# Optimization experiments

Hardware: AMD Instinct MI355X
Metric: run time of the kernel (lower is better)

The kernel has to match this reference:

```python
import jax, jax.numpy as jnp
import numpy as np

N = 50000
NEG_SLOPE = 0.2

def _gat_layer(x, src, dst, W, a_src, a_dst, b):
    # x: [N, Fin], W: [Fin, Fout], a_src/a_dst: [Fout], b: [Fout]
    h = x @ W                                  # [N, Fout]
    alpha_src = h @ a_src                      # [N]
    alpha_dst = h @ a_dst                      # [N]
    e = alpha_src[src] + alpha_dst[dst]        # [E]
    e = jnp.where(e > 0, e, NEG_SLOPE * e)     # leaky_relu
    # segment softmax over incoming edges of each dst node
    m = jax.ops.segment_max(e, dst, num_segments=N)
    w = jnp.exp(e - m[dst])
    denom = jax.ops.segment_sum(w, dst, num_segments=N) + jnp.asarray(1e-16, e.dtype)
    alpha = w / denom[dst]                     # [E]
    out = jax.ops.segment_sum(alpha[:, None] * h[src], dst, num_segments=N)
    return out + b

def setup_inputs() -> dict:
    key = jax.random.key(0)
    ks = jax.random.split(key, 10)
    x = jax.random.normal(ks[0], (N, 128), dtype=jnp.float32)
    edge_index = jax.random.randint(ks[1], (2, 800000), 0, N, dtype=jnp.int64)
    def glorot(k, shape):
        fan = shape[0] + (shape[1] if len(shape) > 1 else 1)
        s = jnp.sqrt(6.0 / fan)
        return jax.random.uniform(k, shape, jnp.float32, -s, s)
    return {
        "x": x,
        "edge_index": edge_index,
        "W1": glorot(ks[2], (128, 64)),
        "a1_src": glorot(ks[3], (64,)),
        "a1_dst": glorot(ks[4], (64,)),
        "b1": jnp.zeros((64,), jnp.float32),
        "W2": glorot(ks[5], (64, 64)),
        "a2_src": glorot(ks[6], (64,)),
        "a2_dst": glorot(ks[7], (64,)),
        "b2": jnp.zeros((64,), jnp.float32),
    }

def reference(x, edge_index, W1, a1_src, a1_dst, b1, W2, a2_src, a2_dst, b2):
    loops = jnp.arange(N, dtype=edge_index.dtype)
    src = jnp.concatenate([edge_index[0], loops])  # add self-loops (PyG default)
    dst = jnp.concatenate([edge_index[1], loops])
    h = _gat_layer(x, src, dst, W1, a1_src, a1_dst, b1)
    h = jax.nn.relu(h)
    out = _gat_layer(h, src, dst, W2, a2_src, a2_dst, b2)
    return out
```

## Files before the change

### kernel.cpp

```cpp
#include <hip/hip_runtime.h>
#include <hip/hip_bf16.h>
#include <hip/hip_fp16.h>
#include <cstddef>


#define NNODES 50000
#define NEDGES 800000
#define FOUT   64
#define NBKT   512
#define BSPAN  98
#define CHUNK  8192
#define REGS   2560
#define NLBMAX 128

__device__ __forceinline__ float leaky(float t) { return t > 0.f ? t : 0.2f * t; }
#define RL(v, j) __builtin_amdgcn_readlane((v), (j))


__global__ __launch_bounds__(256) void k_localsort(
    const int* __restrict__ ei, unsigned* __restrict__ gout,
    int* __restrict__ goff, int E)
{
    __shared__ unsigned lrec[CHUNK];
    __shared__ unsigned lsrt[CHUNK];
    __shared__ int cnt[NBKT];
    __shared__ int cur[NBKT];
    __shared__ int exc[NBKT + 1];

    const int t = threadIdx.x;
    const int blk = blockIdx.x;
    const int e0 = blk * CHUNK;
    const int e1 = min(e0 + CHUNK, E);
    const int ne = e1 - e0;

    for (int i = t; i < NBKT; i += 256) cnt[i] = 0;
    __syncthreads();

    for (int i = e0 + t; i < e1; i += 256) {
        unsigned s = (unsigned)ei[i];
        unsigned d = (unsigned)ei[E + i];
        lrec[i - e0] = s | (d << 16);
        atomicAdd(&cnt[d / BSPAN], 1);
    }
    __syncthreads();

    if (t < 64) {
        int c[8]; int s = 0;
        #pragma unroll
        for (int k = 0; k < 8; ++k) { c[k] = cnt[t * 8 + k]; s += c[k]; }
        int inc = s;
        #pragma unroll
        for (int d = 1; d < 64; d <<= 1) { int u = __shfl_up(inc, d); if (t >= d) inc += u; }
        int ex = inc - s;
        #pragma unroll
        for (int k = 0; k < 8; ++k) { exc[t * 8 + k] = ex; cur[t * 8 + k] = ex; ex += c[k]; }
        if (t == 63) exc[NBKT] = ex;
    }
    __syncthreads();

    for (int i = t; i < ne; i += 256) {
        unsigned r = lrec[i];
        unsigned d = r >> 16;
        unsigned b = d / BSPAN;
        int p = atomicAdd(&cur[b], 1);
        lsrt[p] = (r & 0xFFFFu) | ((d - b * BSPAN) << 16);
    }
    __syncthreads();

    for (int i = t; i < ne; i += 256) gout[e0 + i] = lsrt[i];
    for (int i = t; i < NBKT + 1; i += 256)
        goff[blk * (NBKT + 1) + i] = e0 + exc[i];
}


__global__ __launch_bounds__(256) void k_csr_bucket(
    const unsigned* __restrict__ gout, const int* __restrict__ goff,
    int* __restrict__ csrc, int* __restrict__ rowstart, int* __restrict__ rowend,
    int n, int nlb)
{
    __shared__ unsigned ltmp[REGS];
    __shared__ int lout[REGS];
    __shared__ int lcnt[BSPAN];
    __shared__ int lbase[BSPAN + 1];
    __shared__ int lcur[BSPAN];
    __shared__ int rg0[NLBMAX];
    __shared__ int rbase[NLBMAX + 1];

    const int t = threadIdx.x;
    const int bkt = blockIdx.x;
    const int node0 = bkt * BSPAN;
    if (node0 >= n) return;
    const int nn = min(BSPAN, n - node0);

    for (int i = t; i < BSPAN; i += 256) lcnt[i] = (i < nn) ? 1 : 0;
    __shared__ int rlen[NLBMAX];
    if (t < nlb) {
        int g0 = goff[t * (NBKT + 1) + bkt];
        int g1 = goff[t * (NBKT + 1) + bkt + 1];
        rg0[t] = g0;
        rlen[t] = g1 - g0;
    }
    __syncthreads();

    if (t < 64) {
        int b0 = t * 2, b1 = t * 2 + 1;
        int c0 = (b0 < nlb) ? rlen[b0] : 0;
        int c1 = (b1 < nlb) ? rlen[b1] : 0;
        int s = c0 + c1;
        int inc = s;
        #pragma unroll
        for (int d = 1; d < 64; d <<= 1) { int u = __shfl_up(inc, d); if (t >= d) inc += u; }
        int ex = inc - s;
        rbase[b0] = ex;
        if (b1 <= NLBMAX) rbase[b1] = ex + c0;
        if (t == 63) rbase[nlb] = inc;
    }
    __syncthreads();

    const int tot = min(rbase[nlb], REGS - BSPAN);

    for (int i = t; i < tot; i += 256) {
        int lo = 0, hi = nlb;
        while (hi - lo > 1) {
            int mid = (lo + hi) >> 1;
            if (rbase[mid] <= i) lo = mid; else hi = mid;
        }
        ltmp[i] = gout[rg0[lo] + (i - rbase[lo])];
    }
    __syncthreads();

    for (int i = t; i < tot; i += 256) atomicAdd(&lcnt[ltmp[i] >> 16], 1);
    __syncthreads();

    if (t < 64) {
        int b0 = t * 2, b1 = t * 2 + 1;
        int c0 = (b0 < BSPAN) ? lcnt[b0] : 0;
        int c1 = (b1 < BSPAN) ? lcnt[b1] : 0;
        int s = c0 + c1;
        int inc = s;
        #pragma unroll
        for (int d = 1; d < 64; d <<= 1) { int u = __shfl_up(inc, d); if (t >= d) inc += u; }
        int ex = inc - s;
        if (b0 < BSPAN) { lbase[b0] = ex;      lcur[b0] = ex + 1; }
        if (b1 < BSPAN) { lbase[b1] = ex + c0; lcur[b1] = ex + c0 + 1; }
        if (t == 63) lbase[BSPAN] = inc;
    }
    __syncthreads();

    for (int i = t; i < nn; i += 256) lout[lbase[i]] = node0 + i;
    for (int i = t; i < tot; i += 256) {
        unsigned r = ltmp[i];
        int p = atomicAdd(&lcur[r >> 16], 1);
        lout[p] = (int)(r & 0xFFFFu);
    }
    __syncthreads();

    const int gbase = bkt * REGS;
    const int total = tot + nn;
    for (int i = t; i < total; i += 256) csrc[gbase + i] = lout[i];
    for (int i = t; i < nn; i += 256) {
        rowstart[node0 + i] = gbase + lbase[i];
        rowend[node0 + i]   = gbase + lbase[i + 1];
    }
}


template <int K>
__global__ __launch_bounds__(256) void gemm_alpha(
    const float* __restrict__ x, const float* __restrict__ W,
    const float* __restrict__ a_src, const float* __restrict__ a_dst,
    __half* __restrict__ h16, float* __restrict__ as_, float* __restrict__ ad_, int n)
{
    __shared__ __align__(16) float Ws[K * 64];
    __shared__ __align__(16) float xT[K * 64];
    __shared__ float red_s[4][64];
    __shared__ float red_d[4][64];

    const int t = threadIdx.x;
    const int lane = t & 63;
    const int wv = t >> 6;
    const int rg = lane & 15;
    const int cg = lane >> 4;
    const int r0 = blockIdx.x * 64;
    const int c0 = wv * 16 + cg * 4;

    {
        const float4* Wg = (const float4*)W;
        float4* Wl = (float4*)Ws;
        for (int i = t; i < K * 16; i += 256) Wl[i] = Wg[i];
    }
    for (int i = t; i < 16 * K; i += 256) {
        int r = i & 63;
        int kq = i >> 6;
        int row = r0 + r;
        float4 v = make_float4(0.f, 0.f, 0.f, 0.f);
        if (row < n) v = ((const float4*)(x + (size_t)row * K))[kq];
        xT[(kq * 4 + 0) * 64 + r] = v.x;
        xT[(kq * 4 + 1) * 64 + r] = v.y;
        xT[(kq * 4 + 2) * 64 + r] = v.z;
        xT[(kq * 4 + 3) * 64 + r] = v.w;
    }
    __syncthreads();

    float acc[4][4];
    #pragma unroll
    for (int i = 0; i < 4; ++i)
        #pragma unroll
        for (int j = 0; j < 4; ++j) acc[i][j] = 0.f;

    #pragma unroll 4
    for (int k = 0; k < K; ++k) {
        float4 xa = *(const float4*)&xT[k * 64 + rg * 4];
        float4 wb = *(const float4*)&Ws[k * 64 + c0];
        acc[0][0] = fmaf(xa.x, wb.x, acc[0][0]);
        acc[0][1] = fmaf(xa.x, wb.y, acc[0][1]);
        acc[0][2] = fmaf(xa.x, wb.z, acc[0][2]);
        acc[0][3] = fmaf(xa.x, wb.w, acc[0][3]);
        acc[1][0] = fmaf(xa.y, wb.x, acc[1][0]);
        acc[1][1] = fmaf(xa.y, wb.y, acc[1][1]);
        acc[1][2] = fmaf(xa.y, wb.z, acc[1][2]);
        acc[1][3] = fmaf(xa.y, wb.w, acc[1][3]);
        acc[2][0] = fmaf(xa.z, wb.x, acc[2][0]);
        acc[2][1] = fmaf(xa.z, wb.y, acc[2][1]);
        acc[2][2] = fmaf(xa.z, wb.z, acc[2][2]);
        acc[2][3] = fmaf(xa.z, wb.w, acc[2][3]);
        acc[3][0] = fmaf(xa.w, wb.x, acc[3][0]);
        acc[3][1] = fmaf(xa.w, wb.y, acc[3][1]);
        acc[3][2] = fmaf(xa.w, wb.z, acc[3][2]);
        acc[3][3] = fmaf(xa.w, wb.w, acc[3][3]);
    }

    #pragma unroll
    for (int i = 0; i < 4; ++i) {
        int row = r0 + rg * 4 + i;
        if (row < n) {
            __half2 p0 = __floats2half2_rn(acc[i][0], acc[i][1]);
            __half2 p1 = __floats2half2_rn(acc[i][2], acc[i][3]);
            int2 pk;
            pk.x = *(int*)&p0;
            pk.y = *(int*)&p1;
            *(int2*)(h16 + (size_t)row * 64 + c0) = pk;
        }
    }

    float a_s[4], a_d[4];
    #pragma unroll
    for (int j = 0; j < 4; ++j) { a_s[j] = a_src[c0 + j]; a_d[j] = a_dst[c0 + j]; }
    #pragma unroll
    for (int i = 0; i < 4; ++i) {
        float pa = acc[i][0] * a_s[0] + acc[i][1] * a_s[1] + acc[i][2] * a_s[2] + acc[i][3] * a_s[3];
        float pd = acc[i][0] * a_d[0] + acc[i][1] * a_d[1] + acc[i][2] * a_d[2] + acc[i][3] * a_d[3];
        pa += __shfl_xor(pa, 16); pa += __shfl_xor(pa, 32);
        pd += __shfl_xor(pd, 16); pd += __shfl_xor(pd, 32);
        if (cg == 0) { red_s[wv][rg * 4 + i] = pa; red_d[wv][rg * 4 + i] = pd; }
    }
    __syncthreads();
    if (t < 64) {
        int row = r0 + t;
        if (row < n) {
            as_[row] = red_s[0][t] + red_s[1][t] + red_s[2][t] + red_s[3][t];
            ad_[row] = red_d[0][t] + red_d[1][t] + red_d[2][t] + red_d[3][t];
        }
    }
}


template <bool RELU>
__device__ __forceinline__ void agg_one(
    int node, int lane, int2* __restrict__ swrow,
    const int* __restrict__ rowstart, const int* __restrict__ rowend,
    const int* __restrict__ csrc, const __half* __restrict__ h16,
    const float* __restrict__ as_, const float* __restrict__ ad_,
    const float* __restrict__ bias, float* __restrict__ out)
{
    const int start = rowstart[node];
    const int end   = rowend[node];
    const int deg   = end - start;
    const float adn = ad_[node];

    if (deg <= 64) {
        int s = 0;
        float e = -1e30f;
        if (lane < deg) {
            s = csrc[start + lane];
            e = leaky(as_[s] + adn);
        }
        float m = e;
        #pragma unroll
        for (int d = 32; d >= 1; d >>= 1) m = fmaxf(m, __shfl_xor(m, d));
        float w = (lane < deg) ? __expf(e - m) : 0.f;
        float dsum = w;
        #pragma unroll
        for (int d = 32; d >= 1; d >>= 1) dsum += __shfl_xor(dsum, d);

        swrow[lane] = make_int2(s << 6, __float_as_int(w));

        const int g  = lane >> 3;
        const int fl = (lane & 7) << 3;
        const __half* __restrict__ hf = h16 + fl;
        const int niter = (deg + 7) >> 3;

        int2 sw[8];
        uint4 v[8];
        #pragma unroll
        for (int j = 0; j < 8; ++j) {
            if (j < niter) {
                sw[j] = swrow[(j << 3) + g];
                v[j] = *(const uint4*)(hf + sw[j].x);
            }
        }
        float af[8] = {0.f, 0.f, 0.f, 0.f, 0.f, 0.f, 0.f, 0.f};
        #pragma unroll
        for (int j = 0; j < 8; ++j) {
            if (j < niter) {
                float wj = __int_as_float(sw[j].y);
                unsigned uu[4] = {v[j].x, v[j].y, v[j].z, v[j].w};
                #pragma unroll
                for (int q = 0; q < 4; ++q) {
                    __half2 h2 = *(__half2*)&uu[q];
                    float2 f2 = __half22float2(h2);
                    af[2 * q]     = fmaf(wj, f2.x, af[2 * q]);
                    af[2 * q + 1] = fmaf(wj, f2.y, af[2 * q + 1]);
                }
            }
        }
        #pragma unroll
        for (int q = 0; q < 8; ++q) {
            af[q] += __shfl_xor(af[q], 8);
            af[q] += __shfl_xor(af[q], 16);
            af[q] += __shfl_xor(af[q], 32);
        }
        if (g == 0) {
            float inv = 1.f / dsum;
            float* op = out + (size_t)node * 64 + fl;
            float4 b0 = *(const float4*)(bias + fl);
            float4 b1 = *(const float4*)(bias + fl + 4);
            float4 o0, o1;
            o0.x = fmaf(af[0], inv, b0.x); o0.y = fmaf(af[1], inv, b0.y);
            o0.z = fmaf(af[2], inv, b0.z); o0.w = fmaf(af[3], inv, b0.w);
            o1.x = fmaf(af[4], inv, b1.x); o1.y = fmaf(af[5], inv, b1.y);
            o1.z = fmaf(af[6], inv, b1.z); o1.w = fmaf(af[7], inv, b1.w);
            if (RELU) {
                o0.x = fmaxf(o0.x, 0.f); o0.y = fmaxf(o0.y, 0.f);
                o0.z = fmaxf(o0.z, 0.f); o0.w = fmaxf(o0.w, 0.f);
                o1.x = fmaxf(o1.x, 0.f); o1.y = fmaxf(o1.y, 0.f);
                o1.z = fmaxf(o1.z, 0.f); o1.w = fmaxf(o1.w, 0.f);
            }
            *(float4*)op = o0;
            *(float4*)(op + 4) = o1;
        }
    } else {
        const __half* __restrict__ hp = h16 + lane;
        float m = -1e30f;
        for (int base = start; base < end; base += 64) {
            int idx = base + lane;
            if (idx < end) m = fmaxf(m, leaky(as_[csrc[idx]] + adn));
        }
        #pragma unroll
        for (int d = 32; d >= 1; d >>= 1) m = fmaxf(m, __shfl_xor(m, d));

        float acc0 = 0.f, acc1 = 0.f, acc2 = 0.f, acc3 = 0.f, dsum = 0.f;
        for (int base = start; base < end; base += 64) {
            int idx = base + lane;
            int s = 0; float w = 0.f;
            if (idx < end) {
                s = csrc[idx];
                w = __expf(leaky(as_[s] + adn) - m);
            }
            dsum += w;
            int off = s << 6;
            int wu = __float_as_uint(w);
            int cnt = min(64, end - base);
            int cr = (cnt + 3) & ~3;
            for (int j = 0; j < cr; j += 4) {
                int   o0 = RL(off, j + 0), o1 = RL(off, j + 1);
                int   o2 = RL(off, j + 2), o3 = RL(off, j + 3);
                float w0 = __uint_as_float(RL(wu, j + 0));
                float w1 = __uint_as_float(RL(wu, j + 1));
                float w2 = __uint_as_float(RL(wu, j + 2));
                float w3 = __uint_as_float(RL(wu, j + 3));
                float v0 = __half2float(hp[o0]), v1 = __half2float(hp[o1]);
                float v2 = __half2float(hp[o2]), v3 = __half2float(hp[o3]);
                acc0 = fmaf(w0, v0, acc0);
                acc1 = fmaf(w1, v1, acc1);
                acc2 = fmaf(w2, v2, acc2);
                acc3 = fmaf(w3, v3, acc3);
            }
        }
        #pragma unroll
        for (int d = 32; d >= 1; d >>= 1) dsum += __shfl_xor(dsum, d);
        float acc = (acc0 + acc1) + (acc2 + acc3);
        float o = acc / dsum + bias[lane];
        if (RELU) o = fmaxf(o, 0.f);
        out[(size_t)node * 64 + lane] = o;
    }
}

template <bool RELU>
__global__ __launch_bounds__(256) void k_aggregate(
    const int* __restrict__ rowstart, const int* __restrict__ rowend,
    const int* __restrict__ csrc,
    const __half* __restrict__ h16, const float* __restrict__ as_,
    const float* __restrict__ ad_, const float* __restrict__ bias,
    float* __restrict__ out, int n)
{
    __shared__ int2 swL[4][64];

    const int lane = threadIdx.x & 63;
    const int wid  = threadIdx.x >> 6;
    const int nodeA = (blockIdx.x * 4 + wid) * 2;
    if (nodeA >= n) return;

    const int half = lane >> 5;
    const int hl   = lane & 31;
    const int node = nodeA + half;

    const int start = rowstart[node];
    const int end   = rowend[node];
    const int deg   = end - start;
    const int mdeg  = max(deg, __shfl_xor(deg, 32));

    if (mdeg <= 32) {
        const float adn = ad_[node];
        int s = 0;
        float e = -1e30f;
        if (hl < deg) {
            s = csrc[start + hl];
            e = leaky(as_[s] + adn);
        }
        float m = e;
        #pragma unroll
        for (int d = 16; d >= 1; d >>= 1) m = fmaxf(m, __shfl_xor(m, d));
        float w = (hl < deg) ? __expf(e - m) : 0.f;
        float dsum = w;
        #pragma unroll
        for (int d = 16; d >= 1; d >>= 1) dsum += __shfl_xor(dsum, d);

        swL[wid][lane] = make_int2(s << 6, __float_as_int(w));

        const int g  = (lane >> 3) & 3;
        const int fl = (lane & 7) << 3;
        const __half* __restrict__ hf = h16 + fl;
        int nit = (deg + 3) >> 2;
        nit = max(nit, __shfl_xor(nit, 32));

        const int sbase = (half << 5) + g;
        int2 sw[8];
        uint4 v[8];
        #pragma unroll
        for (int j = 0; j < 8; ++j) {
            if (j < nit) {
                sw[j] = swL[wid][sbase + (j << 2)];
                v[j] = *(const uint4*)(hf + sw[j].x);
            }
        }
        float af[8] = {0.f, 0.f, 0.f, 0.f, 0.f, 0.f, 0.f, 0.f};
        #pragma unroll
        for (int j = 0; j < 8; ++j) {
            if (j < nit) {
                float wj = __int_as_float(sw[j].y);
                unsigned uu[4] = {v[j].x, v[j].y, v[j].z, v[j].w};
                #pragma unroll
                for (int q = 0; q < 4; ++q) {
                    __half2 h2 = *(__half2*)&uu[q];
                    float2 f2 = __half22float2(h2);
                    af[2 * q]     = fmaf(wj, f2.x, af[2 * q]);
                    af[2 * q + 1] = fmaf(wj, f2.y, af[2 * q + 1]);
                }
            }
        }
        #pragma unroll
        for (int q = 0; q < 8; ++q) {
            af[q] += __shfl_xor(af[q], 8);
            af[q] += __shfl_xor(af[q], 16);
        }
        if (g == 0) {
            float inv = 1.f / dsum;
            float* op = out + (size_t)node * 64 + fl;
            float4 b0 = *(const float4*)(bias + fl);
            float4 b1 = *(const float4*)(bias + fl + 4);
            float4 o0, o1;
            o0.x = fmaf(af[0], inv, b0.x); o0.y = fmaf(af[1], inv, b0.y);
            o0.z = fmaf(af[2], inv, b0.z); o0.w = fmaf(af[3], inv, b0.w);
            o1.x = fmaf(af[4], inv, b1.x); o1.y = fmaf(af[5], inv, b1.y);
            o1.z = fmaf(af[6], inv, b1.z); o1.w = fmaf(af[7], inv, b1.w);
            if (RELU) {
                o0.x = fmaxf(o0.x, 0.f); o0.y = fmaxf(o0.y, 0.f);
                o0.z = fmaxf(o0.z, 0.f); o0.w = fmaxf(o0.w, 0.f);
                o1.x = fmaxf(o1.x, 0.f); o1.y = fmaxf(o1.y, 0.f);
                o1.z = fmaxf(o1.z, 0.f); o1.w = fmaxf(o1.w, 0.f);
            }
            *(float4*)op = o0;
            *(float4*)(op + 4) = o1;
        }
    } else {
        agg_one<RELU>(nodeA,     lane, swL[wid], rowstart, rowend, csrc, h16, as_, ad_, bias, out);
        agg_one<RELU>(nodeA + 1, lane, swL[wid], rowstart, rowend, csrc, h16, as_, ad_, bias, out);
    }
}


extern "C" void kernel_launch(void* const* d_in, const int* in_sizes, int n_in,
                              void* d_out, int out_size, void* d_ws, size_t ws_size,
                              hipStream_t stream) {
    const float* x   = (const float*)d_in[0];
    const int*   ei  = (const int*)  d_in[1];
    const float* W1  = (const float*)d_in[2];
    const float* a1s = (const float*)d_in[3];
    const float* a1d = (const float*)d_in[4];
    const float* b1  = (const float*)d_in[5];
    const float* W2  = (const float*)d_in[6];
    const float* a2s = (const float*)d_in[7];
    const float* a2d = (const float*)d_in[8];
    const float* b2  = (const float*)d_in[9];
    float* out = (float*)d_out;

    const int N_ = NNODES, E_ = NEDGES;
    const int NLB = (E_ + CHUNK - 1) / CHUNK;

    char* ws = (char*)d_ws;
    size_t off = 0;
    auto alloc = [&](size_t bytes) -> void* {
        void* p = ws + off;
        off += (bytes + 255) & ~(size_t)255;
        return p;
    };
    int*    csrc     = (int*)alloc((size_t)NBKT * REGS * 4);
    int*    rowstart = (int*)alloc((size_t)N_ * 4);
    int*    rowend   = (int*)alloc((size_t)N_ * 4);
    float*  as_      = (float*)alloc((size_t)N_ * 4);
    float*  ad_      = (float*)alloc((size_t)N_ * 4);
    __half* h16      = (__half*)alloc((size_t)N_ * FOUT * 2);
    unsigned* gout   = (unsigned*)h16;
    int*      goff   = (int*)((char*)h16 + (size_t)NLB * CHUNK * 4);
    float*    xr2    = out;

    k_localsort<<<NLB, 256, 0, stream>>>(ei, gout, goff, E_);
    k_csr_bucket<<<NBKT, 256, 0, stream>>>(gout, goff, csrc, rowstart, rowend, N_, NLB);

    const int GB = (N_ + 63) / 64;
    const int AB = (N_ / 2 + 3) / 4;

    gemm_alpha<128><<<GB, 256, 0, stream>>>(x, W1, a1s, a1d, h16, as_, ad_, N_);
    k_aggregate<true><<<AB, 256, 0, stream>>>(rowstart, rowend, csrc, h16, as_, ad_, b1, xr2, N_);
    gemm_alpha<64><<<GB, 256, 0, stream>>>(xr2, W2, a2s, a2d, h16, as_, ad_, N_);
    k_aggregate<false><<<AB, 256, 0, stream>>>(rowstart, rowend, csrc, h16, as_, ad_, b2, out, N_);
}
```

Before: 191.2 us.

## Replace scalar FP32 GEMM with fp16 MFMA 16x16x32 matrix-core GEMM

```diff
diff --git a/kernel.cpp b/kernel.cpp
--- a/kernel.cpp
+++ b/kernel.cpp
@@ -15,6 +15,10 @@
 
 __device__ __forceinline__ float leaky(float t) { return t > 0.f ? t : 0.2f * t; }
 #define RL(v, j) __builtin_amdgcn_readlane((v), (j))
+
+using half8  = __attribute__((ext_vector_type(8))) _Float16;
+using half4v = __attribute__((ext_vector_type(4))) _Float16;
+using f32x4  = __attribute__((ext_vector_type(4))) float;
 
 
 __global__ __launch_bounds__(256) void k_localsort(
@@ -166,100 +170,93 @@
 
 
 template <int K>
-__global__ __launch_bounds__(256) void gemm_alpha(
+__global__ __launch_bounds__(256) void k_gemm_mfma(
     const float* __restrict__ x, const float* __restrict__ W,
     const float* __restrict__ a_src, const float* __restrict__ a_dst,
     __half* __restrict__ h16, float* __restrict__ as_, float* __restrict__ ad_, int n)
 {
-    __shared__ __align__(16) float Ws[K * 64];
-    __shared__ __align__(16) float xT[K * 64];
-    __shared__ float red_s[4][64];
-    __shared__ float red_d[4][64];
-
-    const int t = threadIdx.x;
+    constexpr int KP = K + 8;
+    __shared__ __align__(16) _Float16 Ah[64 * KP];
+    __shared__ __align__(16) _Float16 Wf[K * 64];
+
+    const int t    = threadIdx.x;
     const int lane = t & 63;
-    const int wv = t >> 6;
-    const int rg = lane & 15;
-    const int cg = lane >> 4;
-    const int r0 = blockIdx.x * 64;
-    const int c0 = wv * 16 + cg * 4;
-
-    {
-        const float4* Wg = (const float4*)W;
-        float4* Wl = (float4*)Ws;
-        for (int i = t; i < K * 16; i += 256) Wl[i] = Wg[i];
-    }
-    for (int i = t; i < 16 * K; i += 256) {
-        int r = i & 63;
-        int kq = i >> 6;
+    const int wv   = t >> 6;
+    const int n16  = lane & 15;
+    const int quad = lane >> 4;
+    const int r0   = blockIdx.x * 64;
+
+    for (int i = t; i < K * 64; i += 256) {
+        int k = i >> 6, c = i & 63;
+        Wf[((k >> 3) * 64 + c) * 8 + (k & 7)] = (_Float16)W[i];
+    }
+    constexpr int KQ = K / 4;
+    for (int i = t; i < 64 * KQ; i += 256) {
+        int r = i / KQ, kq = i % KQ;
         int row = r0 + r;
         float4 v = make_float4(0.f, 0.f, 0.f, 0.f);
         if (row < n) v = ((const float4*)(x + (size_t)row * K))[kq];
-        xT[(kq * 4 + 0) * 64 + r] = v.x;
-        xT[(kq * 4 + 1) * 64 + r] = v.y;
-        xT[(kq * 4 + 2) * 64 + r] = v.z;
-        xT[(kq * 4 + 3) * 64 + r] = v.w;
-    }
-    __syncthreads();
-
-    float acc[4][4];
-    #pragma unroll
-    for (int i = 0; i < 4; ++i)
-        #pragma unroll
-        for (int j = 0; j < 4; ++j) acc[i][j] = 0.f;
-
-    #pragma unroll 4
-    for (int k = 0; k < K; ++k) {
-        float4 xa = *(const float4*)&xT[k * 64 + rg * 4];
-        float4 wb = *(const float4*)&Ws[k * 64 + c0];
-        acc[0][0] = fmaf(xa.x, wb.x, acc[0][0]);
-        acc[0][1] = fmaf(xa.x, wb.y, acc[0][1]);
-        acc[0][2] = fmaf(xa.x, wb.z, acc[0][2]);
-        acc[0][3] = fmaf(xa.x, wb.w, acc[0][3]);
-        acc[1][0] = fmaf(xa.y, wb.x, acc[1][0]);
-        acc[1][1] = fmaf(xa.y, wb.y, acc[1][1]);
-        acc[1][2] = fmaf(xa.y, wb.z, acc[1][2]);
-        acc[1][3] = fmaf(xa.y, wb.w, acc[1][3]);
-        acc[2][0] = fmaf(xa.z, wb.x, acc[2][0]);
-        acc[2][1] = fmaf(xa.z, wb.y, acc[2][1]);
-        acc[2][2] = fmaf(xa.z, wb.z, acc[2][2]);
-        acc[2][3] = fmaf(xa.z, wb.w, acc[2][3]);
-        acc[3][0] = fmaf(xa.w, wb.x, acc[3][0]);
-        acc[3][1] = fmaf(xa.w, wb.y, acc[3][1]);
-        acc[3][2] = fmaf(xa.w, wb.z, acc[3][2]);
-        acc[3][3] = fmaf(xa.w, wb.w, acc[3][3]);
-    }
-
-    #pragma unroll
-    for (int i = 0; i < 4; ++i) {
-        int row = r0 + rg * 4 + i;
-        if (row < n) {
-            __half2 p0 = __floats2half2_rn(acc[i][0], acc[i][1]);
-            __half2 p1 = __floats2half2_rn(acc[i][2], acc[i][3]);
-            int2 pk;
-            pk.x = *(int*)&p0;
-            pk.y = *(int*)&p1;
-            *(int2*)(h16 + (size_t)row * 64 + c0) = pk;
-        }
-    }
-
-    float a_s[4], a_d[4];
-    #pragma unroll
-    for (int j = 0; j < 4; ++j) { a_s[j] = a_src[c0 + j]; a_d[j] = a_dst[c0 + j]; }
-    #pragma unroll
-    for (int i = 0; i < 4; ++i) {
-        float pa = acc[i][0] * a_s[0] + acc[i][1] * a_s[1] + acc[i][2] * a_s[2] + acc[i][3] * a_s[3];
-        float pd = acc[i][0] * a_d[0] + acc[i][1] * a_d[1] + acc[i][2] * a_d[2] + acc[i][3] * a_d[3];
-        pa += __shfl_xor(pa, 16); pa += __shfl_xor(pa, 32);
-        pd += __shfl_xor(pd, 16); pd += __shfl_xor(pd, 32);
-        if (cg == 0) { red_s[wv][rg * 4 + i] = pa; red_d[wv][rg * 4 + i] = pd; }
-    }
-    __syncthreads();
-    if (t < 64) {
-        int row = r0 + t;
-        if (row < n) {
-            as_[row] = red_s[0][t] + red_s[1][t] + red_s[2][t] + red_s[3][t];
-            ad_[row] = red_d[0][t] + red_d[1][t] + red_d[2][t] + red_d[3][t];
+        half4v hv = { (_Float16)v.x, (_Float16)v.y, (_Float16)v.z, (_Float16)v.w };
+        *(half4v*)&Ah[r * KP + kq * 4] = hv;
+    }
+    __syncthreads();
+
+    half8 bfr[K / 32][4];
+    #pragma unroll
+    for (int kk = 0; kk < K / 32; ++kk)
+        #pragma unroll
+        for (int ct = 0; ct < 4; ++ct)
+            bfr[kk][ct] = *(const half8*)&Wf[((kk * 4 + quad) * 64 + ct * 16 + n16) * 8];
+
+    f32x4 acc[4];
+    #pragma unroll
+    for (int ct = 0; ct < 4; ++ct) acc[ct] = (f32x4){0.f, 0.f, 0.f, 0.f};
+
+    #pragma unroll
+    for (int kk = 0; kk < K / 32; ++kk) {
+        half8 a = *(const half8*)&Ah[(wv * 16 + n16) * KP + kk * 32 + quad * 8];
+        #pragma unroll
+        for (int ct = 0; ct < 4; ++ct)
+            acc[ct] = __builtin_amdgcn_mfma_f32_16x16x32_f16(a, bfr[kk][ct], acc[ct], 0, 0, 0);
+    }
+
+    const int rowb = r0 + wv * 16 + quad * 4;
+    float asv[4], adv[4];
+    #pragma unroll
+    for (int ct = 0; ct < 4; ++ct) {
+        asv[ct] = a_src[ct * 16 + n16];
+        adv[ct] = a_dst[ct * 16 + n16];
+    }
+    float pa[4] = {0.f, 0.f, 0.f, 0.f}, pd[4] = {0.f, 0.f, 0.f, 0.f};
+    #pragma unroll
+    for (int ct = 0; ct < 4; ++ct)
+        #pragma unroll
+        for (int r = 0; r < 4; ++r) {
+            pa[r] = fmaf(acc[ct][r], asv[ct], pa[r]);
+            pd[r] = fmaf(acc[ct][r], adv[ct], pd[r]);
+        }
+    #pragma unroll
+    for (int r = 0; r < 4; ++r) {
+        #pragma unroll
+        for (int d = 1; d <= 8; d <<= 1) {
+            pa[r] += __shfl_xor(pa[r], d);
+            pd[r] += __shfl_xor(pd[r], d);
+        }
+    }
+    if (n16 == 0) {
+        #pragma unroll
+        for (int r = 0; r < 4; ++r) {
+            if (rowb + r < n) { as_[rowb + r] = pa[r]; ad_[rowb + r] = pd[r]; }
+        }
+    }
+
+    _Float16* hh = (_Float16*)h16;
+    #pragma unroll
+    for (int r = 0; r < 4; ++r) {
+        if (rowb + r < n) {
+            #pragma unroll
+            for (int ct = 0; ct < 4; ++ct)
+                hh[(size_t)(rowb + r) * 64 + ct * 16 + n16] = (_Float16)acc[ct][r];
         }
     }
 }
@@ -541,8 +538,8 @@
     const int GB = (N_ + 63) / 64;
     const int AB = (N_ / 2 + 3) / 4;
 
-    gemm_alpha<128><<<GB, 256, 0, stream>>>(x, W1, a1s, a1d, h16, as_, ad_, N_);
+    k_gemm_mfma<128><<<GB, 256, 0, stream>>>(x, W1, a1s, a1d, h16, as_, ad_, N_);
     k_aggregate<true><<<AB, 256, 0, stream>>>(rowstart, rowend, csrc, h16, as_, ad_, b1, xr2, N_);
-    gemm_alpha<64><<<GB, 256, 0, stream>>>(xr2, W2, a2s, a2d, h16, as_, ad_, N_);
+    k_gemm_mfma<64><<<GB, 256, 0, stream>>>(xr2, W2, a2s, a2d, h16, as_, ad_, N_);
     k_aggregate<false><<<AB, 256, 0, stream>>>(rowstart, rowend, csrc, h16, as_, ad_, b2, out, N_);
 }
```

Result: faster. 172.7 us (-9.7%).
